# Kernel tuning notes

Measured on AMD Instinct MI355X. Metric: run time of the kernel, lower is better.

## Reference

```python
import math
import jax, jax.numpy as jnp
import numpy as np

B, C, H, W = 2, 256, 256, 256
TH, TW = 256, 256
U = V = 2            # window_size
PE_DIM = 256
DIM = 256
HEADS = 8
TEMP = 10000.0


def sine_pe(y, x, num_pos_feats, temp, card):
    """Faithful port of get_sine_position_encoding (use_norm=True)."""
    eps = 1e-6
    scale = 2.0 * math.pi
    y = y / (card[0] + eps) * scale
    x = x / (card[1] + eps) * scale
    dt = jnp.arange(num_pos_feats, dtype=jnp.float32)
    dim_t = temp ** (2.0 * jnp.floor(dt / 2.0) / num_pos_feats)
    px = x[..., None] / dim_t
    py = y[..., None] / dim_t

    def interleave(p):
        s = jnp.stack((jnp.sin(p[..., 0::2]), jnp.cos(p[..., 1::2])), axis=-1)
        return s.reshape(s.shape[:-2] + (-1,))

    return jnp.concatenate((interleave(py), interleave(px)), axis=-1)


def setup_inputs() -> dict:
    key = jax.random.key(0)
    ks = jax.random.split(key, 8)
    return {
        "feat_supp": jax.random.normal(ks[0], (B, C, H, W), jnp.float32),
        "offset": jax.random.normal(ks[1], (B, TH, TW, 2), jnp.float32) * 2.0,
        "Wq": jax.random.normal(ks[2], (DIM, PE_DIM), jnp.float32) * 0.02,
        "bq": jax.random.normal(ks[3], (DIM,), jnp.float32) * 0.02,
        "Wk": jax.random.normal(ks[4], (DIM, PE_DIM), jnp.float32) * 0.02,
        "bk": jax.random.normal(ks[5], (DIM,), jnp.float32) * 0.02,
        "Wv": jax.random.normal(ks[6], (DIM, PE_DIM), jnp.float32) * 0.02,
        "bv": jax.random.normal(ks[7], (DIM,), jnp.float32) * 0.02,
    }


def reference(feat_supp, offset, Wq, bq, Wk, bk, Wv, bv):
    UV = U * V
    THW = TH * TW
    Dh = DIM // HEADS
    attn_scale = Dh ** (-0.5)
    d = PE_DIM // C  # = 1 here

    # --- warp grid: integer window corners + fractional residual ---
    tgt = jnp.stack(jnp.meshgrid(jnp.arange(TH), jnp.arange(TW), indexing='ij'), axis=-1)  # [TH,TW,2]
    win = jnp.stack(jnp.meshgrid(jnp.arange(U), jnp.arange(V), indexing='ij'), axis=-1)    # [U,V,2]
    full = tgt[None].astype(jnp.float32) + offset[..., ::-1]            # [B,TH,TW,2]
    intg = jnp.floor(full).astype(jnp.int32)
    deci = (full - intg.astype(full.dtype)).reshape(B, THW, 2)          # fractional part
    idx = (intg[:, :, :, None, None, :] + win[None, None, None]).reshape(B, THW * UV, 2)

    # --- duplicate-padding gather (gather_hw) ---
    h_idx = jnp.clip(idx[..., 0], 0, H - 1)
    w_idx = jnp.clip(idx[..., 1], 0, W - 1)
    feat = feat_supp.transpose(0, 2, 3, 1).reshape(B, H * W, C)
    lin = h_idx * W + w_idx                                             # [B, THW*UV]
    feat_warp = jnp.take_along_axis(feat, lin[:, :, None], axis=1)      # [B, THW*UV, C]
    feat_warp_ori = feat_warp.reshape(B, THW, UV, C, 1)

    # --- sine PE on window coords (card = window_size - 1) ---
    ye, xe = jnp.meshgrid(jnp.arange(U, dtype=jnp.float32), jnp.arange(V, dtype=jnp.float32), indexing='ij')
    pos_bias = sine_pe(ye.reshape(1, -1), xe.reshape(1, -1), PE_DIM // 2, TEMP, (U - 1, V - 1))  # [1,UV,PE_DIM]
    pe_warp = pos_bias.reshape(1, 1, UV, C, d)
    fw = (feat_warp_ori + pe_warp).reshape(B, THW, UV, PE_DIM)

    # --- query features: window mean + sine PE of fractional offset (card = window_size) ---
    feat_base = feat_warp_ori[..., 0].mean(axis=2)                      # [B,THW,C]
    pe_curr = sine_pe(deci[..., 0], deci[..., 1], PE_DIM // 2, TEMP, (U, V)).reshape(B, THW, C, d)
    fb = (feat_base[..., None] + pe_curr).reshape(B, THW, PE_DIM)

    # --- cross attention: 1 query vs UV keys per target pixel ---
    q = (fb @ Wq.T + bq).reshape(B, THW, HEADS, Dh)
    k = (fw @ Wk.T + bk).reshape(B, THW, UV, HEADS, Dh)
    v = (fw @ Wv.T + bv).reshape(B, THW, UV, HEADS, Dh)
    attn = jnp.einsum('bthd,btuhd->bthu', q * attn_scale, k)
    attn = jax.nn.softmax(attn, axis=-1)
    out = jnp.einsum('bthu,btuhd->bthd', attn, v).reshape(B, TH, TW, DIM)
    return out.transpose(0, 3, 1, 2)                                    # [B, DIM, TH, TW]
```

## Files before the change

kernel.cpp:

```cpp
#include <hip/hip_runtime.h>


using short8 = __attribute__((ext_vector_type(8))) short;
using uint4v = __attribute__((ext_vector_type(4))) unsigned;
using f32x4  = __attribute__((ext_vector_type(4))) float;
typedef unsigned short u16;

#define LOG2_1E4 13.287712379549449f
#define TWO_PI   6.283185307179586f
#define ATT_SCL  0.17677669529663687f

__device__ __forceinline__ float bs2f(u16 s) {
    unsigned u = ((unsigned)s) << 16;
    float f; __builtin_memcpy(&f, &u, 4); return f;
}
__device__ __forceinline__ u16 f2bs(float f) {
    unsigned u; __builtin_memcpy(&u, &f, 4);
    u += 0x7fffu + ((u >> 16) & 1u);
    return (u16)(u >> 16);
}
__device__ __forceinline__ unsigned cvt_pk_bf16(float lo, float hi) {
    unsigned r;
    asm("v_cvt_pk_bf16_f32 %0, %1, %2" : "=v"(r) : "v"(lo), "v"(hi));
    return r;
}

__device__ __forceinline__ int probe_is_f32(const u16* offs_raw) {
    const int lane = threadIdx.x & 63;
    const float v = bs2f(offs_raw[lane * 2]);
    const float av = fabsf(v);
    const bool insane = !(av >= 1e-3f && av <= 1000.0f);
    return __popcll(__ballot(insane)) >= 16 ? 1 : 0;
}

__global__ __launch_bounds__(256) void irm_canon(
    const void* offs_raw, const void* Wq_r, const void* bq_r,
    const void* Wk_r, const void* bk_r, const void* Wv_r, const void* bv_r,
    unsigned char* canon)
{
    const int is_f32 = probe_is_f32((const u16*)offs_raw);
    float* offsC = (float*)canon;
    u16* WqC = (u16*)(canon + (1u << 20));
    u16* WkC = (u16*)(canon + (1u << 20) + (1u << 17));
    u16* WvC = (u16*)(canon + (1u << 20) + (2u << 17));
    u16* bqC = (u16*)(canon + (1u << 20) + (3u << 17));
    u16* bkC = bqC + 256;
    u16* bvC = bkC + 256;

    const int gid = blockIdx.x * 256 + threadIdx.x;
    if (gid < 262144) {
        offsC[gid] = is_f32 ? ((const float*)offs_raw)[gid]
                            : bs2f(((const u16*)offs_raw)[gid]);
    } else if (gid < 262144 + 3 * 65536) {
        const int r = gid - 262144, w = r >> 16, i = r & 65535;
        const void* src = (w == 0) ? Wq_r : (w == 1) ? Wk_r : Wv_r;
        u16*       dst  = (w == 0) ? WqC  : (w == 1) ? WkC  : WvC;
        dst[i] = is_f32 ? f2bs(((const float*)src)[i]) : ((const u16*)src)[i];
    } else if (gid < 262144 + 3 * 65536 + 3 * 256) {
        const int r = gid - 262144 - 3 * 65536, w = r >> 8, i = r & 255;
        const void* src = (w == 0) ? bq_r : (w == 1) ? bk_r : bv_r;
        u16*       dst  = (w == 0) ? bqC  : (w == 1) ? bkC  : bvC;
        dst[i] = is_f32 ? f2bs(((const float*)src)[i]) : ((const u16*)src)[i];
    }
}

__global__ __launch_bounds__(256) void irm_transpose(const void* __restrict__ feat_raw,
                                                     const u16* __restrict__ offs_raw,
                                                     u16* __restrict__ featT) {
    const int is_f32 = probe_is_f32(offs_raw);
    __shared__ u16 tile[64][72];
    const int b   = blockIdx.z;
    const int c0  = blockIdx.y << 6;
    const int hw0 = blockIdx.x << 6;
    const int tid = threadIdx.x;
    const int r    = tid >> 4;
    const int col4 = (tid & 15) << 2;
    #pragma unroll
    for (int it = 0; it < 4; ++it) {
        const int c = (it << 4) + r;
        const size_t idx = ((size_t)((b << 8) + c0 + c) << 16) + hw0 + col4;
        ushort4 o;
        if (is_f32) {
            const float4 v = *(const float4*)((const float*)feat_raw + idx);
            const unsigned lo = cvt_pk_bf16(v.x, v.y);
            const unsigned hi = cvt_pk_bf16(v.z, v.w);
            o.x = (u16)(lo & 0xffffu); o.y = (u16)(lo >> 16);
            o.z = (u16)(hi & 0xffffu); o.w = (u16)(hi >> 16);
        } else {
            o = *(const ushort4*)((const u16*)feat_raw + idx);
        }
        *(ushort4*)&tile[c][col4 ^ (((c >> 3) & 7) << 3)] = o;
    }
    __syncthreads();
    const int s = tid & 7;
    const int m = tid >> 3;
    #pragma unroll
    for (int it2 = 0; it2 < 2; ++it2) {
        const int hw = (it2 << 5) + m;
        short8 o;
        #pragma unroll
        for (int k = 0; k < 8; ++k) {
            const int c = (s << 3) + k;
            o[k] = (short)tile[c][hw ^ (((c >> 3) & 7) << 3)];
        }
        u16* dst = featT + (((size_t)((b << 16) + hw0 + hw)) << 8) + c0 + (s << 3);
        *(short8*)dst = o;
    }
}

__global__ __launch_bounds__(256, 4) void irm_main(
    const void* __restrict__ fsrc,
    const int transposed,
    const u16* __restrict__ offs_raw,
    const float* __restrict__ offsC,
    const u16* __restrict__ Wq, const u16* __restrict__ bq,
    const u16* __restrict__ Wk, const u16* __restrict__ bk_unused,
    const u16* __restrict__ Wv, const u16* __restrict__ bv,
    void* __restrict__ out_raw)
{
    const int is_f32 = probe_is_f32(offs_raw);

    __shared__ __align__(16) unsigned char smem[40960];
    u16* sFb = (u16*)smem;
    u16* sFw = (u16*)(smem + 8192);

    const int tid = threadIdx.x;
    const int raw = blockIdx.x;
    const int wq_ = ((raw & 7) << 10) | (raw >> 3);
    const int b   = wq_ >> 12;
    const int t0  = (wq_ & 4095) << 4;

    const int lane = tid & 63;
    const int wv   = tid >> 6;
    const int c15  = lane & 15;
    const int qd   = lane >> 4;
    const int colbase = wv << 6;

    const int p0 = tid >> 4;
    const int cx = tid & 15;
    const int t  = t0 + p0;
    const float offx = offsC[((((size_t)b << 16) + (size_t)t) << 1) + 0];
    const float offy = offsC[((((size_t)b << 16) + (size_t)t) << 1) + 1];

    {
        const int ty = t >> 8, tx = t & 255;
        const float fy = (float)ty + offy;
        const float fx = (float)tx + offx;
        const float fiy = floorf(fy), fix = floorf(fx);
        const int iy = (int)fiy, ix = (int)fix;
        const float dy = fy - fiy, dx = fx - fix;

        int lin4[4];
        #pragma unroll
        for (int u = 0; u < 4; ++u) {
            int hy = iy + (u >> 1); hy = hy < 0 ? 0 : (hy > 255 ? 255 : hy);
            int wx = ix + (u & 1);  wx = wx < 0 ? 0 : (wx > 255 ? 255 : wx);
            lin4[u] = (hy << 8) | wx;
        }

        short8 g[4][2];
        if (transposed) {
            #pragma unroll
            for (int u = 0; u < 4; ++u) {
                const u16* src = (const u16*)fsrc +
                    ((((size_t)(b << 16)) + (size_t)lin4[u]) << 8) + (cx << 4);
                g[u][0] = *(const short8*)(src);
                g[u][1] = *(const short8*)(src + 8);
            }
        } else {
            #pragma unroll
            for (int u = 0; u < 4; ++u) {
                #pragma unroll
                for (int i = 0; i < 8; ++i) {
                    const size_t i0 = (((size_t)((b << 8) + (cx << 4) + i)) << 16) + lin4[u];
                    const size_t i1 = (((size_t)((b << 8) + (cx << 4) + 8 + i)) << 16) + lin4[u];
                    g[u][0][i] = is_f32 ? (short)f2bs(((const float*)fsrc)[i0]) : (short)((const u16*)fsrc)[i0];
                    g[u][1][i] = is_f32 ? (short)f2bs(((const float*)fsrc)[i1]) : (short)((const u16*)fsrc)[i1];
                }
            }
        }

        float invt[8], s1[8], c1[8];
        #pragma unroll
        for (int a = 0; a < 8; ++a) {
            const int j = ((cx << 3) + a) & 63;
            invt[a] = exp2f(-(float)j * (LOG2_1E4 / 64.0f));
            const float arg = (TWO_PI / (1.0f + 1e-6f)) * invt[a];
            __sincosf(arg, &s1[a], &c1[a]);
        }

        const bool hi_half = (cx >= 8);
        float gsum[16];
        #pragma unroll
        for (int i = 0; i < 16; ++i) gsum[i] = 0.0f;

        #pragma unroll
        for (int u = 0; u < 4; ++u) {
            const bool sel = hi_half ? (bool)(u & 1) : (bool)(u >> 1);
            unsigned pk[8];
            #pragma unroll
            for (int a = 0; a < 8; ++a) {
                const float f0 = bs2f((u16)g[u][a >> 2][(2 * a) & 7]);
                const float f1 = bs2f((u16)g[u][a >> 2][(2 * a + 1) & 7]);
                gsum[2 * a]     += f0;
                gsum[2 * a + 1] += f1;
                const float w0 = f0 + (sel ? s1[a] : 0.0f);
                const float w1 = f1 + (sel ? c1[a] : 1.0f);
                pk[a] = cvt_pk_bf16(w0, w1);
            }
            const int row = (p0 << 2) + u;
            const int rp  = row ^ (((row >> 3) ^ cx) & 7);
            const uint4v lo = {pk[0], pk[1], pk[2], pk[3]};
            const uint4v hi = {pk[4], pk[5], pk[6], pk[7]};
            *(uint4v*)&sFw[(((2 * cx) * 64 + rp)) * 8]     = lo;
            *(uint4v*)&sFw[(((2 * cx + 1) * 64 + rp)) * 8] = hi;
        }

        const float ys = dy * (TWO_PI / (2.0f + 1e-6f));
        const float xs = dx * (TWO_PI / (2.0f + 1e-6f));
        const float sxy = hi_half ? xs : ys;
        unsigned qk[8];
        #pragma unroll
        for (int a = 0; a < 8; ++a) {
            float s2, c2;
            __sincosf(sxy * invt[a], &s2, &c2);
            qk[a] = cvt_pk_bf16(gsum[2 * a] * 0.25f + s2, gsum[2 * a + 1] * 0.25f + c2);
        }
        const int rb = p0 ^ (cx & 7);
        const uint4v qlo = {qk[0], qk[1], qk[2], qk[3]};
        const uint4v qhi = {qk[4], qk[5], qk[6], qk[7]};
        *(uint4v*)&sFb[((2 * cx) * 16 + rb) * 8]     = qlo;
        *(uint4v*)&sFb[((2 * cx + 1) * 16 + rb) * 8] = qhi;
    }
    __syncthreads();

    const f32x4 zero4 = {0.f, 0.f, 0.f, 0.f};
    const int krow0 = 4 * c15;
    const int kw_hi = (c15 >> 1) & 7;

    #pragma unroll
    for (int h2 = 0; h2 < 2; ++h2) {
        const int ntA = 2 * h2, ntB = 2 * h2 + 1;

        f32x4 accQ[2] = {zero4, zero4};
        #pragma unroll
        for (int half = 0; half < 2; ++half) {
            short8 wf[8];
            #pragma unroll
            for (int i = 0; i < 8; ++i) {
                const int ks = half * 4 + (i >> 1);
                const int nt = (i & 1) ? ntB : ntA;
                wf[i] = *(const short8*)&Wq[(colbase + nt * 16 + c15) * 256 + ks * 32 + qd * 8];
            }
            #pragma unroll
            for (int k4 = 0; k4 < 4; ++k4) {
                const int ks = half * 4 + k4;
                const int gidx = ks * 4 + qd;
                const short8 bfb = *(const short8*)&sFb[(gidx * 16 + (c15 ^ ((gidx >> 1) & 7))) * 8];
                accQ[0] = __builtin_amdgcn_mfma_f32_16x16x32_bf16(wf[k4 * 2 + 0], bfb, accQ[0], 0, 0, 0);
                accQ[1] = __builtin_amdgcn_mfma_f32_16x16x32_bf16(wf[k4 * 2 + 1], bfb, accQ[1], 0, 0, 0);
            }
            __builtin_amdgcn_sched_barrier(0);
        }
        {
            const ushort4 b40 = *(const ushort4*)&bq[colbase + ntA * 16 + qd * 4];
            const ushort4 b41 = *(const ushort4*)&bq[colbase + ntB * 16 + qd * 4];
            accQ[0][0] += bs2f(b40.x); accQ[0][1] += bs2f(b40.y);
            accQ[0][2] += bs2f(b40.z); accQ[0][3] += bs2f(b40.w);
            accQ[1][0] += bs2f(b41.x); accQ[1][1] += bs2f(b41.y);
            accQ[1][2] += bs2f(b41.z); accQ[1][3] += bs2f(b41.w);
        }

        f32x4 accT[4][2];
        #pragma unroll
        for (int u = 0; u < 4; ++u) { accT[u][0] = zero4; accT[u][1] = zero4; }
        #pragma unroll
        for (int half = 0; half < 2; ++half) {
            short8 wf[8];
            #pragma unroll
            for (int i = 0; i < 8; ++i) {
                const int ks = half * 4 + (i >> 1);
                const int nt = (i & 1) ? ntB : ntA;
                wf[i] = *(const short8*)&Wk[(colbase + nt * 16 + c15) * 256 + ks * 32 + qd * 8];
            }
            #pragma unroll
            for (int k4 = 0; k4 < 4; ++k4) {
                const int ks = half * 4 + k4;
                const int gk = ((ks * 4 + qd) >> 1) & 7;
                #pragma unroll
                for (int u = 0; u < 4; ++u) {
                    const int rr = (krow0 + u) ^ (kw_hi ^ gk);
                    const short8 bf = *(const short8*)&sFw[((ks * 4 + qd) * 64 + rr) * 8];
                    accT[u][0] = __builtin_amdgcn_mfma_f32_16x16x32_bf16(wf[k4 * 2 + 0], bf, accT[u][0], 0, 0, 0);
                    accT[u][1] = __builtin_amdgcn_mfma_f32_16x16x32_bf16(wf[k4 * 2 + 1], bf, accT[u][1], 0, 0, 0);
                }
            }
            __builtin_amdgcn_sched_barrier(0);
        }

        float att[4];
        {
            float lg[4];
            #pragma unroll
            for (int u = 0; u < 4; ++u) {
                float acc = 0.0f;
                #pragma unroll
                for (int ntl = 0; ntl < 2; ++ntl)
                    #pragma unroll
                    for (int r = 0; r < 4; ++r)
                        acc += accQ[ntl][r] * accT[u][ntl][r];
                acc += __shfl_xor(acc, 16);
                acc += __shfl_xor(acc, 32);
                lg[u] = acc * ATT_SCL;
            }
            const float mx = fmaxf(fmaxf(lg[0], lg[1]), fmaxf(lg[2], lg[3]));
            float e[4], es = 0.0f;
            #pragma unroll
            for (int u = 0; u < 4; ++u) { e[u] = __expf(lg[u] - mx); es += e[u]; }
            const float inv = __fdividef(1.0f, es);
            #pragma unroll
            for (int u = 0; u < 4; ++u) att[u] = e[u] * inv;
        }
        __builtin_amdgcn_sched_barrier(0);

        #pragma unroll
        for (int u = 0; u < 4; ++u) { accT[u][0] = zero4; accT[u][1] = zero4; }
        #pragma unroll
        for (int half = 0; half < 2; ++half) {
            short8 wf[8];
            #pragma unroll
            for (int i = 0; i < 8; ++i) {
                const int ks = half * 4 + (i >> 1);
                const int nt = (i & 1) ? ntB : ntA;
                wf[i] = *(const short8*)&Wv[(colbase + nt * 16 + c15) * 256 + ks * 32 + qd * 8];
            }
            #pragma unroll
            for (int k4 = 0; k4 < 4; ++k4) {
                const int ks = half * 4 + k4;
                const int gk = ((ks * 4 + qd) >> 1) & 7;
                #pragma unroll
                for (int u = 0; u < 4; ++u) {
                    const int rr = (krow0 + u) ^ (kw_hi ^ gk);
                    const short8 bf = *(const short8*)&sFw[((ks * 4 + qd) * 64 + rr) * 8];
                    accT[u][0] = __builtin_amdgcn_mfma_f32_16x16x32_bf16(wf[k4 * 2 + 0], bf, accT[u][0], 0, 0, 0);
                    accT[u][1] = __builtin_amdgcn_mfma_f32_16x16x32_bf16(wf[k4 * 2 + 1], bf, accT[u][1], 0, 0, 0);
                }
            }
            __builtin_amdgcn_sched_barrier(0);
        }

        #pragma unroll
        for (int ntl = 0; ntl < 2; ++ntl) {
            const int nt = 2 * h2 + ntl;
            const ushort4 bv4 = *(const ushort4*)&bv[colbase + nt * 16 + qd * 4];
            const float bvf[4] = {bs2f(bv4.x), bs2f(bv4.y), bs2f(bv4.z), bs2f(bv4.w)};
            const int cbase = (b << 8) + colbase + nt * 16 + qd * 4;
            #pragma unroll
            for (int r = 0; r < 4; ++r) {
                float val = att[0] * accT[0][ntl][r];
                val += att[1] * accT[1][ntl][r];
                val += att[2] * accT[2][ntl][r];
                val += att[3] * accT[3][ntl][r];
                val += bvf[r];
                if (is_f32) {
                    ((float*)out_raw)[(((size_t)(cbase + r)) << 16) + t0 + c15] = val;
                } else {
                    ((u16*)out_raw)[(((size_t)(cbase + r)) << 16) + t0 + c15] = f2bs(val);
                }
            }
        }
        __builtin_amdgcn_sched_barrier(0);
    }
}

extern "C" void kernel_launch(void* const* d_in, const int* in_sizes, int n_in,
                              void* d_out, int out_size, void* d_ws, size_t ws_size,
                              hipStream_t stream) {
    const size_t FEATT_BYTES = (size_t)1 << 26;
    const size_t CANON_BYTES = (1u << 20) + (3u << 17) + 3 * 512;
    const int use_t = (ws_size >= FEATT_BYTES + CANON_BYTES) ? 1 : 0;

    unsigned char* ws    = (unsigned char*)d_ws;
    unsigned char* canon = ws + (use_t ? FEATT_BYTES : 0);
    float* offsC = (float*)canon;
    u16* WqC = (u16*)(canon + (1u << 20));
    u16* WkC = (u16*)(canon + (1u << 20) + (1u << 17));
    u16* WvC = (u16*)(canon + (1u << 20) + (2u << 17));
    u16* bqC = (u16*)(canon + (1u << 20) + (3u << 17));
    u16* bkC = bqC + 256;
    u16* bvC = bkC + 256;

    irm_canon<<<1795, 256, 0, stream>>>(d_in[1], d_in[2], d_in[3], d_in[4],
                                        d_in[5], d_in[6], d_in[7], canon);
    if (use_t)
        irm_transpose<<<dim3(1024, 4, 2), 256, 0, stream>>>(d_in[0], (const u16*)d_in[1], (u16*)ws);
    irm_main<<<dim3(8192), 256, 0, stream>>>(use_t ? (const void*)ws : d_in[0], use_t,
                                             (const u16*)d_in[1], offsC,
                                             WqC, bqC, WkC, bkC, WvC, bvC, d_out);
}
```

Baseline: 615.7 us.

## Precompute window PE projections through Wk/Wv and hoist Q projection

```diff
diff --git a/kernel.cpp b/kernel.cpp
--- a/kernel.cpp
+++ b/kernel.cpp
@@ -32,6 +32,8 @@
     const bool insane = !(av >= 1e-3f && av <= 1000.0f);
     return __popcll(__ballot(insane)) >= 16 ? 1 : 0;
 }
+
+#define PEW_OFF ((1u << 20) + (3u << 17) + 1536u)
 
 __global__ __launch_bounds__(256) void irm_canon(
     const void* offs_raw, const void* Wq_r, const void* bq_r,
@@ -64,6 +66,35 @@
     }
 }
 
+__global__ __launch_bounds__(256) void irm_pew(
+    const u16* __restrict__ offs_raw, const void* __restrict__ Wk_r,
+    const void* __restrict__ Wv_r, unsigned char* canon)
+{
+    const int is_f32 = probe_is_f32(offs_raw);
+    float* peW = (float*)(canon + PEW_OFF);
+    const int gid = blockIdx.x * 256 + threadIdx.x;
+    const int w = gid >> 10, u = (gid >> 8) & 3, n = gid & 255;
+    const void* W = w ? Wv_r : Wk_r;
+    float acc = 0.0f;
+    for (int c = 0; c < 256; ++c) {
+        const int j = (c & 127) >> 1;
+        const int sel = (c < 128) ? (u >> 1) : (u & 1);
+        float pe;
+        if (sel) {
+            const float invt = exp2f(-(float)j * (LOG2_1E4 / 64.0f));
+            float s, co;
+            __sincosf((TWO_PI / (1.0f + 1e-6f)) * invt, &s, &co);
+            pe = (c & 1) ? co : s;
+        } else {
+            pe = (c & 1) ? 1.0f : 0.0f;
+        }
+        const float wv = is_f32 ? ((const float*)W)[n * 256 + c]
+                                : bs2f(((const u16*)W)[n * 256 + c]);
+        acc += pe * wv;
+    }
+    peW[gid] = acc;
+}
+
 __global__ __launch_bounds__(256) void irm_transpose(const void* __restrict__ feat_raw,
                                                      const u16* __restrict__ offs_raw,
                                                      u16* __restrict__ featT) {
@@ -116,6 +147,7 @@
     const u16* __restrict__ Wq, const u16* __restrict__ bq,
     const u16* __restrict__ Wk, const u16* __restrict__ bk_unused,
     const u16* __restrict__ Wv, const u16* __restrict__ bv,
+    const float* __restrict__ peWk, const float* __restrict__ peWv,
     void* __restrict__ out_raw)
 {
     const int is_f32 = probe_is_f32(offs_raw);
@@ -180,50 +212,33 @@
             }
         }
 
-        float invt[8], s1[8], c1[8];
-        #pragma unroll
-        for (int a = 0; a < 8; ++a) {
-            const int j = ((cx << 3) + a) & 63;
-            invt[a] = exp2f(-(float)j * (LOG2_1E4 / 64.0f));
-            const float arg = (TWO_PI / (1.0f + 1e-6f)) * invt[a];
-            __sincosf(arg, &s1[a], &c1[a]);
-        }
-
-        const bool hi_half = (cx >= 8);
         float gsum[16];
         #pragma unroll
         for (int i = 0; i < 16; ++i) gsum[i] = 0.0f;
-
         #pragma unroll
         for (int u = 0; u < 4; ++u) {
-            const bool sel = hi_half ? (bool)(u & 1) : (bool)(u >> 1);
-            unsigned pk[8];
-            #pragma unroll
-            for (int a = 0; a < 8; ++a) {
-                const float f0 = bs2f((u16)g[u][a >> 2][(2 * a) & 7]);
-                const float f1 = bs2f((u16)g[u][a >> 2][(2 * a + 1) & 7]);
-                gsum[2 * a]     += f0;
-                gsum[2 * a + 1] += f1;
-                const float w0 = f0 + (sel ? s1[a] : 0.0f);
-                const float w1 = f1 + (sel ? c1[a] : 1.0f);
-                pk[a] = cvt_pk_bf16(w0, w1);
+            #pragma unroll
+            for (int i = 0; i < 8; ++i) {
+                gsum[i]     += bs2f((u16)g[u][0][i]);
+                gsum[i + 8] += bs2f((u16)g[u][1][i]);
             }
             const int row = (p0 << 2) + u;
             const int rp  = row ^ (((row >> 3) ^ cx) & 7);
-            const uint4v lo = {pk[0], pk[1], pk[2], pk[3]};
-            const uint4v hi = {pk[4], pk[5], pk[6], pk[7]};
-            *(uint4v*)&sFw[(((2 * cx) * 64 + rp)) * 8]     = lo;
-            *(uint4v*)&sFw[(((2 * cx + 1) * 64 + rp)) * 8] = hi;
-        }
-
+            *(short8*)&sFw[(((2 * cx) * 64 + rp)) * 8]     = g[u][0];
+            *(short8*)&sFw[(((2 * cx + 1) * 64 + rp)) * 8] = g[u][1];
+        }
+
+        const bool hi_half = (cx >= 8);
         const float ys = dy * (TWO_PI / (2.0f + 1e-6f));
         const float xs = dx * (TWO_PI / (2.0f + 1e-6f));
         const float sxy = hi_half ? xs : ys;
         unsigned qk[8];
         #pragma unroll
         for (int a = 0; a < 8; ++a) {
+            const int j = ((cx << 3) + a) & 63;
+            const float invt = exp2f(-(float)j * (LOG2_1E4 / 64.0f));
             float s2, c2;
-            __sincosf(sxy * invt[a], &s2, &c2);
+            __sincosf(sxy * invt, &s2, &c2);
             qk[a] = cvt_pk_bf16(gsum[2 * a] * 0.25f + s2, gsum[2 * a + 1] * 0.25f + c2);
         }
         const int rb = p0 ^ (cx & 7);
@@ -238,81 +253,80 @@
     const int krow0 = 4 * c15;
     const int kw_hi = (c15 >> 1) & 7;
 
+    f32x4 accQt[4];
+    #pragma unroll
+    for (int nt = 0; nt < 4; ++nt) accQt[nt] = zero4;
+    #pragma unroll
+    for (int ks = 0; ks < 8; ++ks) {
+        const int gidx = ks * 4 + qd;
+        const short8 bfb = *(const short8*)&sFb[(gidx * 16 + (c15 ^ ((gidx >> 1) & 7))) * 8];
+        #pragma unroll
+        for (int nt = 0; nt < 4; ++nt) {
+            const short8 aw = *(const short8*)&Wq[(colbase + nt * 16 + c15) * 256 + ks * 32 + qd * 8];
+            accQt[nt] = __builtin_amdgcn_mfma_f32_16x16x32_bf16(aw, bfb, accQt[nt], 0, 0, 0);
+        }
+    }
+    #pragma unroll
+    for (int nt = 0; nt < 4; ++nt) {
+        const ushort4 b4 = *(const ushort4*)&bq[colbase + nt * 16 + qd * 4];
+        accQt[nt][0] += bs2f(b4.x); accQt[nt][1] += bs2f(b4.y);
+        accQt[nt][2] += bs2f(b4.z); accQt[nt][3] += bs2f(b4.w);
+    }
+    __builtin_amdgcn_sched_barrier(0);
+
     #pragma unroll
     for (int h2 = 0; h2 < 2; ++h2) {
         const int ntA = 2 * h2, ntB = 2 * h2 + 1;
 
-        f32x4 accQ[2] = {zero4, zero4};
-        #pragma unroll
-        for (int half = 0; half < 2; ++half) {
-            short8 wf[8];
-            #pragma unroll
-            for (int i = 0; i < 8; ++i) {
-                const int ks = half * 4 + (i >> 1);
-                const int nt = (i & 1) ? ntB : ntA;
-                wf[i] = *(const short8*)&Wq[(colbase + nt * 16 + c15) * 256 + ks * 32 + qd * 8];
-            }
-            #pragma unroll
-            for (int k4 = 0; k4 < 4; ++k4) {
-                const int ks = half * 4 + k4;
-                const int gidx = ks * 4 + qd;
-                const short8 bfb = *(const short8*)&sFb[(gidx * 16 + (c15 ^ ((gidx >> 1) & 7))) * 8];
-                accQ[0] = __builtin_amdgcn_mfma_f32_16x16x32_bf16(wf[k4 * 2 + 0], bfb, accQ[0], 0, 0, 0);
-                accQ[1] = __builtin_amdgcn_mfma_f32_16x16x32_bf16(wf[k4 * 2 + 1], bfb, accQ[1], 0, 0, 0);
-            }
-            __builtin_amdgcn_sched_barrier(0);
-        }
-        {
-            const ushort4 b40 = *(const ushort4*)&bq[colbase + ntA * 16 + qd * 4];
-            const ushort4 b41 = *(const ushort4*)&bq[colbase + ntB * 16 + qd * 4];
-            accQ[0][0] += bs2f(b40.x); accQ[0][1] += bs2f(b40.y);
-            accQ[0][2] += bs2f(b40.z); accQ[0][3] += bs2f(b40.w);
-            accQ[1][0] += bs2f(b41.x); accQ[1][1] += bs2f(b41.y);
-            accQ[1][2] += bs2f(b41.z); accQ[1][3] += bs2f(b41.w);
-        }
-
-        f32x4 accT[4][2];
-        #pragma unroll
-        for (int u = 0; u < 4; ++u) { accT[u][0] = zero4; accT[u][1] = zero4; }
-        #pragma unroll
-        for (int half = 0; half < 2; ++half) {
-            short8 wf[8];
-            #pragma unroll
-            for (int i = 0; i < 8; ++i) {
-                const int ks = half * 4 + (i >> 1);
-                const int nt = (i & 1) ? ntB : ntA;
-                wf[i] = *(const short8*)&Wk[(colbase + nt * 16 + c15) * 256 + ks * 32 + qd * 8];
-            }
-            #pragma unroll
-            for (int k4 = 0; k4 < 4; ++k4) {
-                const int ks = half * 4 + k4;
-                const int gk = ((ks * 4 + qd) >> 1) & 7;
-                #pragma unroll
-                for (int u = 0; u < 4; ++u) {
-                    const int rr = (krow0 + u) ^ (kw_hi ^ gk);
-                    const short8 bf = *(const short8*)&sFw[((ks * 4 + qd) * 64 + rr) * 8];
-                    accT[u][0] = __builtin_amdgcn_mfma_f32_16x16x32_bf16(wf[k4 * 2 + 0], bf, accT[u][0], 0, 0, 0);
-                    accT[u][1] = __builtin_amdgcn_mfma_f32_16x16x32_bf16(wf[k4 * 2 + 1], bf, accT[u][1], 0, 0, 0);
-                }
-            }
-            __builtin_amdgcn_sched_barrier(0);
-        }
-
-        float att[4];
-        {
-            float lg[4];
-            #pragma unroll
-            for (int u = 0; u < 4; ++u) {
+        float lg[4];
+        #pragma unroll
+        for (int up = 0; up < 2; ++up) {
+            f32x4 accK[2][2];
+            accK[0][0] = zero4; accK[0][1] = zero4;
+            accK[1][0] = zero4; accK[1][1] = zero4;
+            #pragma unroll
+            for (int half = 0; half < 2; ++half) {
+                short8 wf[8];
+                #pragma unroll
+                for (int i = 0; i < 8; ++i) {
+                    const int ks = half * 4 + (i >> 1);
+                    const int nt = (i & 1) ? ntB : ntA;
+                    wf[i] = *(const short8*)&Wk[(colbase + nt * 16 + c15) * 256 + ks * 32 + qd * 8];
+                }
+                #pragma unroll
+                for (int k4 = 0; k4 < 4; ++k4) {
+                    const int ks = half * 4 + k4;
+                    const int gk = ((ks * 4 + qd) >> 1) & 7;
+                    #pragma unroll
+                    for (int uu = 0; uu < 2; ++uu) {
+                        const int row = krow0 + 2 * up + uu;
+                        const int rr = row ^ (kw_hi ^ gk);
+                        const short8 bf = *(const short8*)&sFw[((ks * 4 + qd) * 64 + rr) * 8];
+                        accK[uu][0] = __builtin_amdgcn_mfma_f32_16x16x32_bf16(wf[k4 * 2 + 0], bf, accK[uu][0], 0, 0, 0);
+                        accK[uu][1] = __builtin_amdgcn_mfma_f32_16x16x32_bf16(wf[k4 * 2 + 1], bf, accK[uu][1], 0, 0, 0);
+                    }
+                }
+                __builtin_amdgcn_sched_barrier(0);
+            }
+            #pragma unroll
+            for (int uu = 0; uu < 2; ++uu) {
+                const int u = 2 * up + uu;
+                const float4 pk0 = *(const float4*)&peWk[u * 256 + colbase + ntA * 16 + qd * 4];
+                const float4 pk1 = *(const float4*)&peWk[u * 256 + colbase + ntB * 16 + qd * 4];
                 float acc = 0.0f;
                 #pragma unroll
-                for (int ntl = 0; ntl < 2; ++ntl)
-                    #pragma unroll
-                    for (int r = 0; r < 4; ++r)
-                        acc += accQ[ntl][r] * accT[u][ntl][r];
+                for (int r = 0; r < 4; ++r) {
+                    acc += accQt[ntA][r] * (accK[uu][0][r] + ((const float*)&pk0)[r]);
+                    acc += accQt[ntB][r] * (accK[uu][1][r] + ((const float*)&pk1)[r]);
+                }
                 acc += __shfl_xor(acc, 16);
                 acc += __shfl_xor(acc, 32);
                 lg[u] = acc * ATT_SCL;
             }
+        }
+
+        float att[4];
+        {
             const float mx = fmaxf(fmaxf(lg[0], lg[1]), fmaxf(lg[2], lg[3]));
             float e[4], es = 0.0f;
             #pragma unroll
@@ -323,30 +337,48 @@
         }
         __builtin_amdgcn_sched_barrier(0);
 
-        #pragma unroll
-        for (int u = 0; u < 4; ++u) { accT[u][0] = zero4; accT[u][1] = zero4; }
-        #pragma unroll
-        for (int half = 0; half < 2; ++half) {
-            short8 wf[8];
-            #pragma unroll
-            for (int i = 0; i < 8; ++i) {
-                const int ks = half * 4 + (i >> 1);
-                const int nt = (i & 1) ? ntB : ntA;
-                wf[i] = *(const short8*)&Wv[(colbase + nt * 16 + c15) * 256 + ks * 32 + qd * 8];
-            }
-            #pragma unroll
-            for (int k4 = 0; k4 < 4; ++k4) {
-                const int ks = half * 4 + k4;
-                const int gk = ((ks * 4 + qd) >> 1) & 7;
-                #pragma unroll
-                for (int u = 0; u < 4; ++u) {
-                    const int rr = (krow0 + u) ^ (kw_hi ^ gk);
-                    const short8 bf = *(const short8*)&sFw[((ks * 4 + qd) * 64 + rr) * 8];
-                    accT[u][0] = __builtin_amdgcn_mfma_f32_16x16x32_bf16(wf[k4 * 2 + 0], bf, accT[u][0], 0, 0, 0);
-                    accT[u][1] = __builtin_amdgcn_mfma_f32_16x16x32_bf16(wf[k4 * 2 + 1], bf, accT[u][1], 0, 0, 0);
-                }
-            }
-            __builtin_amdgcn_sched_barrier(0);
+        f32x4 outA[2] = {zero4, zero4};
+        #pragma unroll
+        for (int up = 0; up < 2; ++up) {
+            f32x4 accV[2][2];
+            accV[0][0] = zero4; accV[0][1] = zero4;
+            accV[1][0] = zero4; accV[1][1] = zero4;
+            #pragma unroll
+            for (int half = 0; half < 2; ++half) {
+                short8 wf[8];
+                #pragma unroll
+                for (int i = 0; i < 8; ++i) {
+                    const int ks = half * 4 + (i >> 1);
+                    const int nt = (i & 1) ? ntB : ntA;
+                    wf[i] = *(const short8*)&Wv[(colbase + nt * 16 + c15) * 256 + ks * 32 + qd * 8];
+                }
+                #pragma unroll
+                for (int k4 = 0; k4 < 4; ++k4) {
+                    const int ks = half * 4 + k4;
+                    const int gk = ((ks * 4 + qd) >> 1) & 7;
+                    #pragma unroll
+                    for (int uu = 0; uu < 2; ++uu) {
+                        const int row = krow0 + 2 * up + uu;
+                        const int rr = row ^ (kw_hi ^ gk);
+                        const short8 bf = *(const short8*)&sFw[((ks * 4 + qd) * 64 + rr) * 8];
+                        accV[uu][0] = __builtin_amdgcn_mfma_f32_16x16x32_bf16(wf[k4 * 2 + 0], bf, accV[uu][0], 0, 0, 0);
+                        accV[uu][1] = __builtin_amdgcn_mfma_f32_16x16x32_bf16(wf[k4 * 2 + 1], bf, accV[uu][1], 0, 0, 0);
+                    }
+                }
+                __builtin_amdgcn_sched_barrier(0);
+            }
+            #pragma unroll
+            for (int uu = 0; uu < 2; ++uu) {
+                const int u = 2 * up + uu;
+                const float a = att[u];
+                const float4 pv0 = *(const float4*)&peWv[u * 256 + colbase + ntA * 16 + qd * 4];
+                const float4 pv1 = *(const float4*)&peWv[u * 256 + colbase + ntB * 16 + qd * 4];
+                #pragma unroll
+                for (int r = 0; r < 4; ++r) {
+                    outA[0][r] += a * (accV[uu][0][r] + ((const float*)&pv0)[r]);
+                    outA[1][r] += a * (accV[uu][1][r] + ((const float*)&pv1)[r]);
+                }
+            }
         }
 
         #pragma unroll
@@ -357,11 +389,7 @@
             const int cbase = (b << 8) + colbase + nt * 16 + qd * 4;
             #pragma unroll
             for (int r = 0; r < 4; ++r) {
-                float val = att[0] * accT[0][ntl][r];
-                val += att[1] * accT[1][ntl][r];
-                val += att[2] * accT[2][ntl][r];
-                val += att[3] * accT[3][ntl][r];
-                val += bvf[r];
+                const float val = outA[ntl][r] + bvf[r];
                 if (is_f32) {
                     ((float*)out_raw)[(((size_t)(cbase + r)) << 16) + t0 + c15] = val;
                 } else {
@@ -377,7 +405,7 @@
                               void* d_out, int out_size, void* d_ws, size_t ws_size,
                               hipStream_t stream) {
     const size_t FEATT_BYTES = (size_t)1 << 26;
-    const size_t CANON_BYTES = (1u << 20) + (3u << 17) + 3 * 512;
+    const size_t CANON_BYTES = PEW_OFF + 8192;
     const int use_t = (ws_size >= FEATT_BYTES + CANON_BYTES) ? 1 : 0;
 
     unsigned char* ws    = (unsigned char*)d_ws;
@@ -389,12 +417,16 @@
     u16* bqC = (u16*)(canon + (1u << 20) + (3u << 17));
     u16* bkC = bqC + 256;
     u16* bvC = bkC + 256;
+    float* peWkC = (float*)(canon + PEW_OFF);
+    float* peWvC = peWkC + 1024;
 
     irm_canon<<<1795, 256, 0, stream>>>(d_in[1], d_in[2], d_in[3], d_in[4],
                                         d_in[5], d_in[6], d_in[7], canon);
+    irm_pew<<<8, 256, 0, stream>>>((const u16*)d_in[1], d_in[4], d_in[6], canon);
     if (use_t)
         irm_transpose<<<dim3(1024, 4, 2), 256, 0, stream>>>(d_in[0], (const u16*)d_in[1], (u16*)ws);
     irm_main<<<dim3(8192), 256, 0, stream>>>(use_t ? (const void*)ws : d_in[0], use_t,
                                              (const u16*)d_in[1], offsC,
-                                             WqC, bqC, WkC, bkC, WvC, bvC, d_out);
-}
+                                             WqC, bqC, WkC, bkC, WvC, bvC,
+                                             peWkC, peWvC, d_out);
+}
```

New measurement: 891.8 us. 44.8% more time.
